# Kernel optimization log

Measured on AMD Instinct MI355X. Metric: run time of the kernel, lower is better.

Reference implementation:

```python
import jax, jax.numpy as jnp
import numpy as np

B, T, S, E, H, D = 4, 1024, 1024, 1024, 16, 64


def _ln(x, g, b, eps=1e-5):
    m = x.mean(-1, keepdims=True)
    v = ((x - m) ** 2).mean(-1, keepdims=True)
    return (x - m) * jax.lax.rsqrt(v + eps) * g + b


def _mha(xq, xkv, mask4, Wq, Wk, Wv, Wo, bo):
    # Wq/Wk/Wv: [H, E, D] (stacked per-head bias-free linears)
    q = jnp.einsum('bte,hed->bhtd', xq, Wq)
    k = jnp.einsum('bse,hed->bhsd', xkv, Wk)
    v = jnp.einsum('bse,hed->bhsd', xkv, Wv)
    # NOTE: original scales by C**-0.5 with C = n_embd, not head_size
    wei = jnp.einsum('bhtd,bhsd->bhts', q, k) * (float(E) ** -0.5)
    wei = jnp.where(mask4 == 0, jnp.float32(-1e9), wei)
    wei = jax.nn.softmax(wei, axis=-1)
    o = jnp.einsum('bhts,bhsd->bhtd', wei, v)  # [B,H,T,D]
    b_, h_, t_, d_ = o.shape
    o = o.transpose(0, 2, 1, 3).reshape(b_, t_, h_ * d_)
    return o @ Wo + bo


def setup_inputs() -> dict:
    key = jax.random.key(0)
    ks = jax.random.split(key, 24)
    sd = 0.02
    inp = {
        'x': jax.random.normal(ks[0], (B, T, E), jnp.float32),
        'x_m': jnp.ones((B, 1, T), jnp.int32),
        'ca': jax.random.normal(ks[1], (B, S, E), jnp.float32),
        'ca_m': jnp.ones((B, 1, S), jnp.int32),
        'Wq_s': jax.random.normal(ks[2], (H, E, D), jnp.float32) * sd,
        'Wk_s': jax.random.normal(ks[3], (H, E, D), jnp.float32) * sd,
        'Wv_s': jax.random.normal(ks[4], (H, E, D), jnp.float32) * sd,
        'Wo_s': jax.random.normal(ks[5], (E, E), jnp.float32) * sd,
        'bo_s': jnp.zeros((E,), jnp.float32),
        'Wq_c': jax.random.normal(ks[6], (H, E, D), jnp.float32) * sd,
        'Wk_c': jax.random.normal(ks[7], (H, E, D), jnp.float32) * sd,
        'Wv_c': jax.random.normal(ks[8], (H, E, D), jnp.float32) * sd,
        'Wo_c': jax.random.normal(ks[9], (E, E), jnp.float32) * sd,
        'bo_c': jnp.zeros((E,), jnp.float32),
        'ln1_g': jnp.ones((E,), jnp.float32), 'ln1_b': jnp.zeros((E,), jnp.float32),
        'ln2_g': jnp.ones((E,), jnp.float32), 'ln2_b': jnp.zeros((E,), jnp.float32),
        'ln3_g': jnp.ones((E,), jnp.float32), 'ln3_b': jnp.zeros((E,), jnp.float32),
        'W1': jax.random.normal(ks[10], (E, 4 * E), jnp.float32) * sd,
        'b1': jnp.zeros((4 * E,), jnp.float32),
        'W2': jax.random.normal(ks[11], (4 * E, E), jnp.float32) * sd,
        'b2': jnp.zeros((E,), jnp.float32),
    }
    return inp


def reference(x, x_m, ca, ca_m, Wq_s, Wk_s, Wv_s, Wo_s, bo_s,
              Wq_c, Wk_c, Wv_c, Wo_c, bo_c,
              ln1_g, ln1_b, ln2_g, ln2_b, ln3_g, ln3_b,
              W1, b1, W2, b2):
    tril = jnp.tril(jnp.ones((T, T), jnp.int32))
    # self-attn mask: x_m [B,1,T] & tril [T,T] -> [B,1,T,T] (broadcast over heads)
    self_mask = x_m[:, :, None, :] * tril          # [B,1,T,T]
    cross_mask = ca_m[:, :, None, :]               # [B,1,1,S]
    x = x + _mha(_ln(x, ln1_g, ln1_b), _ln(x, ln1_g, ln1_b) if False else _ln(x, ln1_g, ln1_b), self_mask, Wq_s, Wk_s, Wv_s, Wo_s, bo_s)
    x = x + _mha(_ln(x, ln2_g, ln2_b), ca, cross_mask, Wq_c, Wk_c, Wv_c, Wo_c, bo_c)
    h = _ln(x, ln3_g, ln3_b)
    x = x + (jax.nn.relu(h @ W1 + b1) @ W2 + b2)
    return x
```

## Files before the change

kernel.cpp:

```cpp
#include <hip/hip_runtime.h>
#include <hip/hip_bf16.h>
#include <cstdint>
#include <cstddef>

typedef __attribute__((ext_vector_type(8))) short  s8v;
typedef __attribute__((ext_vector_type(4))) short  s4v;
typedef __attribute__((ext_vector_type(8))) __bf16 b8v;
typedef __attribute__((ext_vector_type(4))) float  f32x4;
typedef __attribute__((ext_vector_type(4))) unsigned u32x4;

#define SC2Q 0.0450843293f

__device__ __forceinline__ short f2bf(float f){
  unsigned u = __builtin_bit_cast(unsigned, f);
  unsigned r = (u + 0x7fffu + ((u >> 16) & 1u)) >> 16;
  return (short)(unsigned short)r;
}
__device__ __forceinline__ float bf2f(short s){
  return __builtin_bit_cast(float, ((unsigned)(unsigned short)s) << 16);
}

__device__ __forceinline__ f32x4 mfma16(s8v a, s8v b, f32x4 c){
  return __builtin_amdgcn_mfma_f32_16x16x32_bf16(
      __builtin_bit_cast(b8v, a), __builtin_bit_cast(b8v, b), c, 0, 0, 0);
}

__device__ __forceinline__ unsigned cvtpk(float a, float b){
  unsigned w;
  asm("v_cvt_pk_bf16_f32 %0, %1, %2" : "=v"(w) : "v"(a), "v"(b));
  return w;
}

__global__ __launch_bounds__(256)
void ln_k(const float* __restrict__ x, const float* __restrict__ g,
          const float* __restrict__ b, short* __restrict__ out)
{
  const int row = blockIdx.x, tid = threadIdx.x;
  const float4 v = ((const float4*)(x + (size_t)row*1024))[tid];
  float s  = v.x+v.y+v.z+v.w;
  float s2 = v.x*v.x+v.y*v.y+v.z*v.z+v.w*v.w;
  #pragma unroll
  for (int off=32; off; off>>=1){ s += __shfl_down(s, off); s2 += __shfl_down(s2, off); }
  __shared__ float red[8];
  const int wave = tid>>6, lane = tid&63;
  if (lane==0){ red[wave]=s; red[4+wave]=s2; }
  __syncthreads();
  s  = red[0]+red[1]+red[2]+red[3];
  s2 = red[4]+red[5]+red[6]+red[7];
  const float mean = s*(1.f/1024.f);
  const float rstd = rsqrtf(s2*(1.f/1024.f) - mean*mean + 1e-5f);
  const float4 gv = ((const float4*)g)[tid];
  const float4 bv = ((const float4*)b)[tid];
  s4v o;
  o[0] = f2bf((v.x-mean)*rstd*gv.x + bv.x);
  o[1] = f2bf((v.y-mean)*rstd*gv.y + bv.y);
  o[2] = f2bf((v.z-mean)*rstd*gv.z + bv.z);
  o[3] = f2bf((v.w-mean)*rstd*gv.w + bv.w);
  *(s4v*)(out + (size_t)row*1024 + tid*4) = o;
}

__global__ __launch_bounds__(256)
void cast_k(const float* __restrict__ in, short* __restrict__ out)
{
  const int i = blockIdx.x*256 + threadIdx.x;
  const float4 v = ((const float4*)in)[i];
  s4v o; o[0]=f2bf(v.x); o[1]=f2bf(v.y); o[2]=f2bf(v.z); o[3]=f2bf(v.w);
  ((s4v*)out)[i] = o;
}

__global__ __launch_bounds__(256)
void mkb_k(const int* __restrict__ xm, const int* __restrict__ cm,
           float* __restrict__ mbS, float* __restrict__ mbC)
{
  const int i = blockIdx.x*256 + threadIdx.x;
  mbS[i] = xm[i] ? 0.f : -1.5e9f;
  mbC[i] = cm[i] ? 0.f : -1.5e9f;
}

__global__ __launch_bounds__(256)
void tcast_k(const float* __restrict__ in, short* __restrict__ out, int E2, int D2)
{
  __shared__ float t[32][33];
  const int h  = blockIdx.z;
  const int e0 = blockIdx.x*32, d0 = blockIdx.y*32;
  const int tx = threadIdx.x & 31, ty = threadIdx.x >> 5;
  const float* ip = in + (size_t)h*E2*D2;
  #pragma unroll
  for (int r = ty; r < 32; r += 8)
    t[r][tx] = ip[(size_t)(e0+r)*D2 + d0 + tx];
  __syncthreads();
  short* op = out + (size_t)h*D2*E2;
  #pragma unroll
  for (int r = ty; r < 32; r += 8)
    op[(size_t)(d0+r)*E2 + e0 + tx] = f2bf(t[tx][r]);
}

__global__ __launch_bounds__(256)
void vtrans_k(const short* __restrict__ V, int ldv, short* __restrict__ Vt, int S, int H)
{
  __shared__ short t[32][34];
  const int bh = blockIdx.z;
  const int b = bh / H, h = bh % H;
  const int s0 = blockIdx.x*32, d0 = blockIdx.y*32;
  const int tx = threadIdx.x & 31, ty = threadIdx.x >> 5;
  const short* ip = V + (size_t)b*S*ldv + h*64;
  #pragma unroll
  for (int r = ty; r < 32; r += 8)
    t[r][tx] = ip[(size_t)(s0+r)*ldv + d0 + tx];
  __syncthreads();
  const int s  = s0 + tx;
  const int ks = (s>>5)&1, bb = (tx>>4)&1, hh = (tx>>2)&3, rr = tx&3;
  const int cp = (s & ~63) + ks*32 + hh*8 + bb*4 + rr;
  short* op = Vt + ((size_t)bh*64 + d0)*S;
  #pragma unroll
  for (int r = ty; r < 32; r += 8)
    op[(size_t)r*S + cp] = t[tx][r];
}

__global__ __launch_bounds__(256)
void red4_k(const short* __restrict__ p, const float* __restrict__ bias,
            const float* __restrict__ resid, float* __restrict__ out)
{
  const int i = blockIdx.x*256 + threadIdx.x;
  float4 o = ((const float4*)resid)[i];
  const float4 bv = ((const float4*)bias)[i & 255];
  o.x += bv.x; o.y += bv.y; o.z += bv.z; o.w += bv.w;
  #pragma unroll
  for (int z=0; z<4; z++){
    const s4v v = ((const s4v*)(p + (size_t)z*4194304))[i];
    o.x += bf2f(v[0]); o.y += bf2f(v[1]); o.z += bf2f(v[2]); o.w += bf2f(v[3]);
  }
  ((float4*)out)[i] = o;
}

template<int BN, int BIAS, int RELU, int RESID, int WF32, int SCQ>
__global__ __launch_bounds__(256, 2)
void gemm_bt(const short* __restrict__ A, const short* __restrict__ Bt,
             const float* __restrict__ bias, const float* __restrict__ resid,
             short* __restrict__ Cb, float* __restrict__ Cf,
             int M, int N, int K)
{
  __shared__ short lds[3][128*32 + BN*32];
  const int nwg = gridDim.x * gridDim.y;
  int id = blockIdx.y * gridDim.x + blockIdx.x;
  id = (id & 7) * (nwg >> 3) + (id >> 3);
  const int bx = id % gridDim.x, by = id / gridDim.x;
  const int m0 = by*128, n0 = bx*BN;

  const int tid  = threadIdx.x;
  const int wave = tid>>6, lane = tid&63;
  const int lo = lane&15, hi = lane>>4;
  const int wm = wave>>1, wn = wave&1;

  constexpr int NJ = BN/32;
  constexpr int BC = BN>>6;
  f32x4 acc[4][NJ] = {};
  const int NK = K >> 5;

  auto stage = [&](int buf, int kt){
    const short* Ag = A  + (size_t)m0*K + kt*32;
    const short* Bg = Bt + (size_t)n0*K + kt*32;
    #pragma unroll
    for (int c=0;c<2;c++){
      const int q = (wave*2+c)*64 + lane;
      const int r = q>>2, cc = q&3;
      __builtin_amdgcn_global_load_lds(
        (const __attribute__((address_space(1))) void*)(Ag + (size_t)r*K + cc*8),
        (__attribute__((address_space(3))) void*)(&lds[buf][(wave*2+c)*512]),
        16, 0, 0);
    }
    #pragma unroll
    for (int c=0;c<BC;c++){
      const int q = (wave*BC+c)*64 + lane;
      const int r = q>>2, cc = q&3;
      __builtin_amdgcn_global_load_lds(
        (const __attribute__((address_space(1))) void*)(Bg + (size_t)r*K + cc*8),
        (__attribute__((address_space(3))) void*)(&lds[buf][4096 + (wave*BC+c)*512]),
        16, 0, 0);
    }
  };

  stage(0, 0);
  if (NK > 1) stage(1, 1);

  for (int kt=0; kt<NK; kt++){
    if (kt+1 < NK){
      if constexpr (BN==128) asm volatile("s_waitcnt vmcnt(4)" ::: "memory");
      else                   asm volatile("s_waitcnt vmcnt(3)" ::: "memory");
    } else {
      asm volatile("s_waitcnt vmcnt(0)" ::: "memory");
    }
    __builtin_amdgcn_s_barrier();
    __builtin_amdgcn_sched_barrier(0);
    if (kt+2 < NK) stage((kt+2)%3, kt+2);

    const short* la = &lds[kt%3][0];
    const short* lb = &lds[kt%3][4096];
    s8v af[4], bfr[NJ];
    #pragma unroll
    for (int i=0;i<4;i++)
      af[i] = *(const s8v*)(la + (wm*64 + i*16 + lo)*32 + hi*8);
    #pragma unroll
    for (int j=0;j<NJ;j++)
      bfr[j] = *(const s8v*)(lb + (wn*(BN/2) + j*16 + lo)*32 + hi*8);
    #pragma unroll
    for (int i=0;i<4;i++)
      #pragma unroll
      for (int j=0;j<NJ;j++)
        acc[i][j] = mfma16(af[i], bfr[j], acc[i][j]);
  }

  #pragma unroll
  for (int i=0;i<4;i++){
    const int row = m0 + wm*64 + i*16 + hi*4;
    #pragma unroll
    for (int j=0;j<NJ;j++){
      const int col = n0 + wn*(BN/2) + j*16 + lo;
      const float bv = BIAS ? bias[col] : 0.0f;
      #pragma unroll
      for (int r=0;r<4;r++){
        float v = acc[i][j][r] + bv;
        if constexpr (SCQ==2) v *= SC2Q;
        if (RELU) v = fmaxf(v, 0.0f);
        const size_t idx = (size_t)(row + r)*N + col;
        if (RESID) v += resid[idx];
        if (WF32) Cf[idx] = v; else Cb[idx] = f2bf(v);
      }
    }
  }
}

template<int BIAS, int RELU, int RESID, int WF32, int SCQ>
__global__ __launch_bounds__(512, 1)
void gemm256(const short* __restrict__ A, int lda,
             const short* __restrict__ Bt, int ldb,
             const float* __restrict__ bias, const float* __restrict__ resid,
             short* __restrict__ Cb, float* __restrict__ Cf,
             int M, int N, int K)
{
  __shared__ short lds[2][32768];
  const int nwg = gridDim.x * gridDim.y;
  int id = blockIdx.y * gridDim.x + blockIdx.x;
  id = (id & 7) * (nwg >> 3) + (id >> 3);
  const int bx = id % gridDim.x, by = id / gridDim.x;
  const int m0 = by*256, n0 = bx*256;
  A  += (size_t)blockIdx.z * K;
  Bt += (size_t)blockIdx.z * K;
  const size_t cofs = (size_t)blockIdx.z * M * N;

  const int tid = threadIdx.x;
  const int lane = tid&63, wave = tid>>6;
  const int lo = lane&15, hi = lane>>4;
  const int wr = wave>>2, wc = wave&3;

  f32x4 acc[8][4] = {};
  const int NT = K >> 6;

  auto stageA = [&](int buf, int kt, int part){
    const short* Ag = A + (size_t)m0*lda + kt*64;
    const int q = part*512 + tid;
    const int r = q>>3, c = q&7;
    __builtin_amdgcn_global_load_lds(
      (const __attribute__((address_space(1))) void*)(Ag + (size_t)r*lda + ((c^(r&7))*8)),
      (__attribute__((address_space(3))) void*)(&lds[buf][q*8]), 16, 0, 0);
  };
  auto stageB = [&](int buf, int kt, int part){
    const short* Bg = Bt + (size_t)n0*ldb + kt*64;
    const int q = part*512 + tid;
    const int r = q>>3, c = q&7;
    __builtin_amdgcn_global_load_lds(
      (const __attribute__((address_space(1))) void*)(Bg + (size_t)r*ldb + ((c^(r&7))*8)),
      (__attribute__((address_space(3))) void*)(&lds[buf][16384 + q*8]), 16, 0, 0);
  };

  #pragma unroll
  for (int p=0;p<4;p++){ stageA(0,0,p); stageB(0,0,p); }
  __syncthreads();

  for (int t=0; t<NT; t++){
    const int cur = t&1;
    const short* la = &lds[cur][0];
    const short* lb = &lds[cur][16384];
    const bool pf = (t+1 < NT);
    #pragma unroll
    for (int ks=0; ks<2; ks++){
      s8v bf[4];
      #pragma unroll
      for (int j=0;j<4;j++){
        const int r = wc*64 + j*16 + lo;
        bf[j] = *(const s8v*)(lb + r*64 + (((ks*4+hi)^(r&7))*8));
      }
      #pragma unroll
      for (int mh=0; mh<2; mh++){
        s8v af[4];
        #pragma unroll
        for (int i=0;i<4;i++){
          const int r = wr*128 + mh*64 + i*16 + lo;
          af[i] = *(const s8v*)(la + r*64 + (((ks*4+hi)^(r&7))*8));
        }
        if (pf && ks==0){
          stageA(cur^1, t+1, mh*2);   stageB(cur^1, t+1, mh*2);
          stageA(cur^1, t+1, mh*2+1); stageB(cur^1, t+1, mh*2+1);
        }
        __builtin_amdgcn_s_setprio(1);
        #pragma unroll
        for (int i=0;i<4;i++)
          #pragma unroll
          for (int j=0;j<4;j++)
            acc[mh*4+i][j] = mfma16(af[i], bf[j], acc[mh*4+i][j]);
        __builtin_amdgcn_s_setprio(0);
      }
    }
    __syncthreads();
  }

  #pragma unroll
  for (int I=0;I<8;I++){
    const int row = m0 + wr*128 + I*16 + hi*4;
    #pragma unroll
    for (int j=0;j<4;j++){
      const int col = n0 + wc*64 + j*16 + lo;
      const float bv = BIAS ? bias[col] : 0.0f;
      #pragma unroll
      for (int r=0;r<4;r++){
        float v = acc[I][j][r] + bv;
        if constexpr (SCQ==1) { if (col < 1024) v *= SC2Q; }
        if (RELU) v = fmaxf(v, 0.0f);
        const size_t idx = cofs + (size_t)(row + r)*N + col;
        if (RESID) v += resid[idx];
        if (WF32) Cf[idx] = v; else Cb[idx] = f2bf(v);
      }
    }
  }
}

template<int CAUSAL>
__global__ __launch_bounds__(256, 4)
void attn_k(const short* __restrict__ Q, int ldq,
            const short* __restrict__ K, int ldk,
            const short* __restrict__ Vt, int ldvt,
            const float* __restrict__ mbias,
            short* __restrict__ O, int ldo,
            int H, int Tq, int Sk)
{
  __shared__ short kls[2][4096];
  __shared__ short vls[2][4096];
  const int bh = blockIdx.x;
  const int b = bh / H, h = bh % H;
  const int tid = threadIdx.x;
  const int wave = tid>>6, lane = tid&63;
  const int lo = lane&15, hi = lane>>4;
  const int t0 = blockIdx.y*64 + wave*16;

  const short* Qb  = Q + (size_t)(b*Tq)*ldq + h*64;
  const short* Kb  = K + (size_t)(b*Sk)*ldk + h*64;
  const short* Vtb = Vt + (size_t)bh*64*ldvt;
  const float* mb  = mbias + (size_t)b*Sk;

  const short* qp = Qb + (size_t)(t0+lo)*ldq + hi*8;
  const s8v qa0 = *(const s8v*)(qp);
  const s8v qa1 = *(const s8v*)(qp + 32);

  float mrow = -INFINITY, lrow = 0.f;
  f32x4 oacc[4] = {};
  const int trow = t0 + lo;
  const int nblk = CAUSAL ? (blockIdx.y + 1) : (Sk>>6);
  const int x8 = lo & 7;

  auto stage = [&](int buf, int it){
    const int s0 = it*64;
    #pragma unroll
    for (int rd=0; rd<2; rd++){
      const int q = rd*256 + tid;
      const int r = q>>3, c = q&7;
      const int cs = (c ^ (r&7))*8;
      __builtin_amdgcn_global_load_lds(
        (const __attribute__((address_space(1))) void*)(Kb + (size_t)(s0+r)*ldk + cs),
        (__attribute__((address_space(3))) void*)(&kls[buf][(rd*256 + wave*64)*8]),
        16, 0, 0);
      __builtin_amdgcn_global_load_lds(
        (const __attribute__((address_space(1))) void*)(Vtb + (size_t)r*ldvt + s0 + cs),
        (__attribute__((address_space(3))) void*)(&vls[buf][(rd*256 + wave*64)*8]),
        16, 0, 0);
    }
  };

  stage(0, 0);
  int cur = 0;
  for (int it=0; it<nblk; it++){
    __syncthreads();
    if (it+1 < nblk) stage(cur^1, it+1);
    const int s0 = it*64;

    const short* kl = kls[cur];
    s8v kf[4][2];
    #pragma unroll
    for (int g=0; g<4; g++){
      const int rb = (g*16 + lo)*64;
      kf[g][0] = *(const s8v*)(kl + rb + ((hi     ^ x8)*8));
      kf[g][1] = *(const s8v*)(kl + rb + (((4+hi) ^ x8)*8));
    }

    f32x4 sg[4] = {};
    __builtin_amdgcn_s_setprio(1);
    #pragma unroll
    for (int g=0; g<4; g++){
      sg[g] = mfma16(kf[g][0], qa0, sg[g]);
      sg[g] = mfma16(kf[g][1], qa1, sg[g]);
    }
    __builtin_amdgcn_s_setprio(0);

    float p[4][4];
    #pragma unroll
    for (int g=0; g<4; g++){
      const f32x4 mv = ((const f32x4*)mb)[(s0>>2) + g*4 + hi];
      #pragma unroll
      for (int r=0; r<4; r++)
        p[g][r] = sg[g][r] + mv[r];
    }
    if (CAUSAL && it == nblk-1){
      #pragma unroll
      for (int g=0; g<4; g++)
        #pragma unroll
        for (int r=0; r<4; r++){
          const int sidx = s0 + g*16 + 4*hi + r;
          if (sidx > trow) p[g][r] = -1.5e9f;
        }
    }

    float bmax;
    {
      const float m0_ = fmaxf(fmaxf(fmaxf(p[0][0],p[0][1]),p[0][2]),p[0][3]);
      const float m1_ = fmaxf(fmaxf(fmaxf(p[1][0],p[1][1]),p[1][2]),p[1][3]);
      const float m2_ = fmaxf(fmaxf(fmaxf(p[2][0],p[2][1]),p[2][2]),p[2][3]);
      const float m3_ = fmaxf(fmaxf(fmaxf(p[3][0],p[3][1]),p[3][2]),p[3][3]);
      bmax = fmaxf(fmaxf(m0_,m1_), fmaxf(m2_,m3_));
    }
    bmax = fmaxf(bmax, __shfl_xor(bmax, 16));
    bmax = fmaxf(bmax, __shfl_xor(bmax, 32));

    if (!__all(bmax <= mrow + 8.0f)){
      const float mn  = fmaxf(mrow, bmax);
      const float fac = exp2f(mrow - mn);
      mrow = mn;
      lrow *= fac;
      #pragma unroll
      for (int f=0; f<4; f++)
        #pragma unroll
        for (int r=0; r<4; r++)
          oacc[f][r] *= fac;
    }

    float bsum;
    {
      #pragma unroll
      for (int g=0; g<4; g++)
        #pragma unroll
        for (int r=0; r<4; r++)
          p[g][r] = exp2f(p[g][r] - mrow);
      const float s0_ = (p[0][0]+p[0][1]) + (p[0][2]+p[0][3]);
      const float s1_ = (p[1][0]+p[1][1]) + (p[1][2]+p[1][3]);
      const float s2_ = (p[2][0]+p[2][1]) + (p[2][2]+p[2][3]);
      const float s3_ = (p[3][0]+p[3][1]) + (p[3][2]+p[3][3]);
      bsum = (s0_+s1_) + (s2_+s3_);
    }
    bsum += __shfl_xor(bsum, 16);
    bsum += __shfl_xor(bsum, 32);
    lrow += bsum;

    u32x4 pw0, pw1;
    pw0[0] = cvtpk(p[0][0], p[0][1]);
    pw0[1] = cvtpk(p[0][2], p[0][3]);
    pw0[2] = cvtpk(p[1][0], p[1][1]);
    pw0[3] = cvtpk(p[1][2], p[1][3]);
    pw1[0] = cvtpk(p[2][0], p[2][1]);
    pw1[1] = cvtpk(p[2][2], p[2][3]);
    pw1[2] = cvtpk(p[3][0], p[3][1]);
    pw1[3] = cvtpk(p[3][2], p[3][3]);
    const s8v pb0 = __builtin_bit_cast(s8v, pw0);
    const s8v pb1 = __builtin_bit_cast(s8v, pw1);

    const short* vl = vls[cur];
    __builtin_amdgcn_s_setprio(1);
    #pragma unroll
    for (int f=0; f<4; f++){
      const int rb = (f*16 + lo)*64;
      const s8v av0 = *(const s8v*)(vl + rb + (((hi  ) ^ x8)*8));
      const s8v av1 = *(const s8v*)(vl + rb + (((4+hi) ^ x8)*8));
      oacc[f] = mfma16(av0, pb0, oacc[f]);
      oacc[f] = mfma16(av1, pb1, oacc[f]);
    }
    __builtin_amdgcn_s_setprio(0);
    cur ^= 1;
  }

  const float inv = 1.0f / lrow;
  short* Ob = O + (size_t)(b*Tq)*ldo + h*64 + (size_t)(t0+lo)*ldo + 4*hi;
  #pragma unroll
  for (int f=0; f<4; f++){
    s4v o;
    #pragma unroll
    for (int r=0; r<4; r++) o[r] = f2bf(oacc[f][r]*inv);
    *(s4v*)(Ob + f*16) = o;
  }
}

extern "C" void kernel_launch(void* const* d_in, const int* in_sizes, int n_in,
                              void* d_out, int out_size, void* d_ws, size_t ws_size,
                              hipStream_t stream)
{
  (void)in_sizes; (void)n_in; (void)out_size; (void)ws_size;
  const float* x    = (const float*)d_in[0];
  const int*   xm   = (const int*)  d_in[1];
  const float* ca   = (const float*)d_in[2];
  const int*   cam  = (const int*)  d_in[3];
  const float* Wq_s = (const float*)d_in[4];
  const float* Wk_s = (const float*)d_in[5];
  const float* Wv_s = (const float*)d_in[6];
  const float* Wo_s = (const float*)d_in[7];
  const float* bo_s = (const float*)d_in[8];
  const float* Wq_c = (const float*)d_in[9];
  const float* Wk_c = (const float*)d_in[10];
  const float* Wv_c = (const float*)d_in[11];
  const float* Wo_c = (const float*)d_in[12];
  const float* bo_c = (const float*)d_in[13];
  const float* ln1g = (const float*)d_in[14];
  const float* ln1b = (const float*)d_in[15];
  const float* ln2g = (const float*)d_in[16];
  const float* ln2b = (const float*)d_in[17];
  const float* ln3g = (const float*)d_in[18];
  const float* ln3b = (const float*)d_in[19];
  const float* W1   = (const float*)d_in[20];
  const float* b1   = (const float*)d_in[21];
  const float* W2   = (const float*)d_in[22];
  const float* b2   = (const float*)d_in[23];
  float* out = (float*)d_out;

  char* ws = (char*)d_ws;
  size_t off = 0;
  auto alloc = [&](size_t bytes)->void*{
    void* p = ws + off; off += (bytes + 255) & ~(size_t)255; return p; };

  short* w_qkv_s = (short*)alloc((size_t)3072*1024*2);
  short* w_o_s   = (short*)alloc((size_t)1024*1024*2);
  short* w_q_c   = (short*)alloc((size_t)1024*1024*2);
  short* w_kv_c  = (short*)alloc((size_t)2048*1024*2);
  short* w_o_c   = (short*)alloc((size_t)1024*1024*2);
  short* w_1     = (short*)alloc((size_t)4096*1024*2);
  short* w_2     = (short*)alloc((size_t)1024*4096*2);
  short* xn      = (short*)alloc((size_t)4096*1024*2);
  short* cab     = (short*)alloc((size_t)4096*1024*2);
  short* qkv     = (short*)alloc((size_t)4096*3072*2);
  short* attno   = (short*)alloc((size_t)4096*1024*2);
  float* xres    = (float*)alloc((size_t)4096*1024*4);
  short* hffn    = (short*)alloc((size_t)4096*4096*2);
  float* pA      = (float*)alloc((size_t)4096*1024*4);
  float* pB      = (float*)alloc((size_t)4096*1024*4);
  float* mbS     = (float*)alloc((size_t)4096*4);
  float* mbC     = (float*)alloc((size_t)4096*4);
  short* pP      = (short*)pA;
  short* kvbuf   = qkv + (size_t)4096*1024;
  short* vt_s    = hffn;
  short* vt_c    = hffn + (size_t)4*1024*1024;
  (void)pB;

  tcast_k<<<dim3(32,  2,16),256,0,stream>>>(Wq_s, w_qkv_s,           1024,   64);
  tcast_k<<<dim3(32,  2,16),256,0,stream>>>(Wk_s, w_qkv_s+1024*1024, 1024,   64);
  tcast_k<<<dim3(32,  2,16),256,0,stream>>>(Wv_s, w_qkv_s+2048*1024, 1024,   64);
  tcast_k<<<dim3(32, 32, 1),256,0,stream>>>(Wo_s, w_o_s,             1024, 1024);
  tcast_k<<<dim3(32,  2,16),256,0,stream>>>(Wq_c, w_q_c,             1024,   64);
  tcast_k<<<dim3(32,  2,16),256,0,stream>>>(Wk_c, w_kv_c,            1024,   64);
  tcast_k<<<dim3(32,  2,16),256,0,stream>>>(Wv_c, w_kv_c+1024*1024,  1024,   64);
  tcast_k<<<dim3(32, 32, 1),256,0,stream>>>(Wo_c, w_o_c,             1024, 1024);
  tcast_k<<<dim3(32,128, 1),256,0,stream>>>(W1,   w_1,               1024, 4096);
  tcast_k<<<dim3(128,32, 1),256,0,stream>>>(W2,   w_2,               4096, 1024);
  cast_k<<<4096,256,0,stream>>>(ca, cab);
  mkb_k<<<16,256,0,stream>>>(xm, cam, mbS, mbC);

  ln_k<<<4096,256,0,stream>>>(x, ln1g, ln1b, xn);
  gemm256<0,0,0,0,1><<<dim3(12,16),512,0,stream>>>(xn, 1024, w_qkv_s, 1024,
                                                   nullptr, nullptr, qkv, nullptr,
                                                   4096, 3072, 1024);
  vtrans_k<<<dim3(32,2,64),256,0,stream>>>(qkv+2048, 3072, vt_s, 1024, 16);
  attn_k<1><<<dim3(64,16),256,0,stream>>>(qkv, 3072, qkv+1024, 3072, vt_s, 1024,
                                          mbS, attno, 1024, 16, 1024, 1024);
  gemm_bt<64,1,0,1,1,0><<<dim3(16,32),256,0,stream>>>(attno, w_o_s, bo_s, x,
                                                      nullptr, xres, 4096, 1024, 1024);

  ln_k<<<4096,256,0,stream>>>(xres, ln2g, ln2b, xn);
  gemm_bt<64,0,0,0,0,2><<<dim3(16,32),256,0,stream>>>(xn, w_q_c, nullptr, nullptr,
                                                      qkv, nullptr, 4096, 1024, 1024);
  gemm256<0,0,0,0,0><<<dim3(8,16),512,0,stream>>>(cab, 1024, w_kv_c, 1024,
                                                  nullptr, nullptr, kvbuf, nullptr,
                                                  4096, 2048, 1024);
  vtrans_k<<<dim3(32,2,64),256,0,stream>>>(kvbuf+1024, 2048, vt_c, 1024, 16);
  attn_k<0><<<dim3(64,16),256,0,stream>>>(qkv, 1024, kvbuf, 2048, vt_c, 1024,
                                          mbC, attno, 1024, 16, 1024, 1024);
  gemm_bt<64,1,0,1,1,0><<<dim3(16,32),256,0,stream>>>(attno, w_o_c, bo_c, xres,
                                                      nullptr, xres, 4096, 1024, 1024);

  ln_k<<<4096,256,0,stream>>>(xres, ln3g, ln3b, xn);
  gemm256<1,1,0,0,0><<<dim3(16,16),512,0,stream>>>(xn, 1024, w_1, 1024,
                                                   b1, nullptr, hffn, nullptr,
                                                   4096, 4096, 1024);
  gemm256<0,0,0,0,0><<<dim3(4,16,4),512,0,stream>>>(hffn, 4096, w_2, 4096,
                                                    nullptr, nullptr, pP, nullptr,
                                                    4096, 1024, 1024);
  red4_k<<<4096,256,0,stream>>>(pP, b2, xres, out);
}
```

Measured before the change: 368.0 us.

## Compute softmax row sums via MFMA with ones vector and precompute staging addresses

Replaces the per-iteration VALU summation and cross-lane shuffles for the softmax denominator with two extra MFMAs that multiply a bf16 ones vector by the probability fragments, accumulating the row sum in a matrix accumulator. It also hoists the global-to-LDS staging addresses into incrementing pointers, and uses byte-offset LDS addressing and a pointer-advanced mask bias load. The max reduction is reordered into a flatter tree. This trades shuffles and scalar adds for extra matrix-core work, and the denominator now sums bf16-rounded probabilities, which slightly changes numerics.

New measurement: 362.4 us. No clear change (-1.5%).

```diff
diff --git a/kernel.cpp b/kernel.cpp
--- a/kernel.cpp
+++ b/kernel.cpp
@@ -355,50 +355,66 @@
   const short* Qb  = Q + (size_t)(b*Tq)*ldq + h*64;
   const short* Kb  = K + (size_t)(b*Sk)*ldk + h*64;
   const short* Vtb = Vt + (size_t)bh*64*ldvt;
-  const float* mb  = mbias + (size_t)b*Sk;
 
   const short* qp = Qb + (size_t)(t0+lo)*ldq + hi*8;
   const s8v qa0 = *(const s8v*)(qp);
   const s8v qa1 = *(const s8v*)(qp + 32);
 
-  float mrow = -INFINITY, lrow = 0.f;
+  float mrow = -INFINITY;
   f32x4 oacc[4] = {};
+  f32x4 oaccL = {};
   const int trow = t0 + lo;
   const int nblk = CAUSAL ? (blockIdx.y + 1) : (Sk>>6);
   const int x8 = lo & 7;
 
-  auto stage = [&](int buf, int it){
-    const int s0 = it*64;
-    #pragma unroll
-    for (int rd=0; rd<2; rd++){
-      const int q = rd*256 + tid;
-      const int r = q>>3, c = q&7;
-      const int cs = (c ^ (r&7))*8;
-      __builtin_amdgcn_global_load_lds(
-        (const __attribute__((address_space(1))) void*)(Kb + (size_t)(s0+r)*ldk + cs),
-        (__attribute__((address_space(3))) void*)(&kls[buf][(rd*256 + wave*64)*8]),
-        16, 0, 0);
-      __builtin_amdgcn_global_load_lds(
-        (const __attribute__((address_space(1))) void*)(Vtb + (size_t)r*ldvt + s0 + cs),
-        (__attribute__((address_space(3))) void*)(&vls[buf][(rd*256 + wave*64)*8]),
-        16, 0, 0);
-    }
+  const s8v onesv = {(short)0x3F80,(short)0x3F80,(short)0x3F80,(short)0x3F80,
+                     (short)0x3F80,(short)0x3F80,(short)0x3F80,(short)0x3F80};
+
+  const int q0 = tid, q1 = 256 + tid;
+  const int r0 = q0>>3, cs0 = ((q0&7) ^ (r0&7))*8;
+  const int r1 = q1>>3, cs1 = ((q1&7) ^ (r1&7))*8;
+  const short* kS0 = Kb + (size_t)r0*ldk + cs0;
+  const short* kS1 = Kb + (size_t)r1*ldk + cs1;
+  const short* vS0 = Vtb + (size_t)r0*ldvt + cs0;
+  const short* vS1 = Vtb + (size_t)r1*ldvt + cs1;
+  const size_t kAdv = (size_t)64*ldk;
+
+  auto stage = [&](int buf){
+    __builtin_amdgcn_global_load_lds(
+      (const __attribute__((address_space(1))) void*)kS0,
+      (__attribute__((address_space(3))) void*)(&kls[buf][wave*512]), 16, 0, 0);
+    __builtin_amdgcn_global_load_lds(
+      (const __attribute__((address_space(1))) void*)kS1,
+      (__attribute__((address_space(3))) void*)(&kls[buf][2048 + wave*512]), 16, 0, 0);
+    __builtin_amdgcn_global_load_lds(
+      (const __attribute__((address_space(1))) void*)vS0,
+      (__attribute__((address_space(3))) void*)(&vls[buf][wave*512]), 16, 0, 0);
+    __builtin_amdgcn_global_load_lds(
+      (const __attribute__((address_space(1))) void*)vS1,
+      (__attribute__((address_space(3))) void*)(&vls[buf][2048 + wave*512]), 16, 0, 0);
+    kS0 += kAdv; kS1 += kAdv; vS0 += 64; vS1 += 64;
   };
 
-  stage(0, 0);
-  int cur = 0;
+  const char* klsB = (const char*)kls;
+  const char* vlsB = (const char*)vls;
+  const int A0 = lo*128 + ((hi     ^ x8)*16);
+  const int A1 = lo*128 + (((4+hi) ^ x8)*16);
+  int curB = 0;
+
+  const char* mbp = (const char*)(mbias + (size_t)b*Sk) + hi*16;
+
+  stage(0);
   for (int it=0; it<nblk; it++){
     __syncthreads();
-    if (it+1 < nblk) stage(cur^1, it+1);
-    const int s0 = it*64;
-
-    const short* kl = kls[cur];
+    if (it+1 < nblk) stage((it+1)&1);
+
+    const char* ka0 = klsB + curB + A0;
+    const char* ka1 = klsB + curB + A1;
     s8v kf[4][2];
     #pragma unroll
     for (int g=0; g<4; g++){
-      const int rb = (g*16 + lo)*64;
-      kf[g][0] = *(const s8v*)(kl + rb + ((hi     ^ x8)*8));
-      kf[g][1] = *(const s8v*)(kl + rb + (((4+hi) ^ x8)*8));
+      kf[g][0] = *(const s8v*)(ka0 + g*2048);
+      kf[g][1] = *(const s8v*)(ka1 + g*2048);
     }
 
     f32x4 sg[4] = {};
@@ -413,12 +429,14 @@
     float p[4][4];
     #pragma unroll
     for (int g=0; g<4; g++){
-      const f32x4 mv = ((const f32x4*)mb)[(s0>>2) + g*4 + hi];
+      const f32x4 mv = *(const f32x4*)(mbp + g*64);
       #pragma unroll
       for (int r=0; r<4; r++)
         p[g][r] = sg[g][r] + mv[r];
     }
+    mbp += 256;
     if (CAUSAL && it == nblk-1){
+      const int s0 = it*64;
       #pragma unroll
       for (int g=0; g<4; g++)
         #pragma unroll
@@ -430,11 +448,12 @@
 
     float bmax;
     {
-      const float m0_ = fmaxf(fmaxf(fmaxf(p[0][0],p[0][1]),p[0][2]),p[0][3]);
-      const float m1_ = fmaxf(fmaxf(fmaxf(p[1][0],p[1][1]),p[1][2]),p[1][3]);
-      const float m2_ = fmaxf(fmaxf(fmaxf(p[2][0],p[2][1]),p[2][2]),p[2][3]);
-      const float m3_ = fmaxf(fmaxf(fmaxf(p[3][0],p[3][1]),p[3][2]),p[3][3]);
-      bmax = fmaxf(fmaxf(m0_,m1_), fmaxf(m2_,m3_));
+      const float m0_ = fmaxf(fmaxf(p[0][0],p[0][1]),p[0][2]);
+      const float m1_ = fmaxf(fmaxf(p[0][3],p[1][0]),p[1][1]);
+      const float m2_ = fmaxf(fmaxf(p[1][2],p[1][3]),p[2][0]);
+      const float m3_ = fmaxf(fmaxf(p[2][1],p[2][2]),p[2][3]);
+      const float m4_ = fmaxf(fmaxf(p[3][0],p[3][1]),p[3][2]);
+      bmax = fmaxf(fmaxf(fmaxf(m0_,m1_),m2_), fmaxf(fmaxf(m3_,m4_),p[3][3]));
     }
     bmax = fmaxf(bmax, __shfl_xor(bmax, 16));
     bmax = fmaxf(bmax, __shfl_xor(bmax, 32));
@@ -443,30 +462,20 @@
       const float mn  = fmaxf(mrow, bmax);
       const float fac = exp2f(mrow - mn);
       mrow = mn;
-      lrow *= fac;
       #pragma unroll
       for (int f=0; f<4; f++)
         #pragma unroll
         for (int r=0; r<4; r++)
           oacc[f][r] *= fac;
-    }
-
-    float bsum;
-    {
-      #pragma unroll
-      for (int g=0; g<4; g++)
-        #pragma unroll
-        for (int r=0; r<4; r++)
-          p[g][r] = exp2f(p[g][r] - mrow);
-      const float s0_ = (p[0][0]+p[0][1]) + (p[0][2]+p[0][3]);
-      const float s1_ = (p[1][0]+p[1][1]) + (p[1][2]+p[1][3]);
-      const float s2_ = (p[2][0]+p[2][1]) + (p[2][2]+p[2][3]);
-      const float s3_ = (p[3][0]+p[3][1]) + (p[3][2]+p[3][3]);
-      bsum = (s0_+s1_) + (s2_+s3_);
-    }
-    bsum += __shfl_xor(bsum, 16);
-    bsum += __shfl_xor(bsum, 32);
-    lrow += bsum;
+      #pragma unroll
+      for (int r=0; r<4; r++) oaccL[r] *= fac;
+    }
+
+    #pragma unroll
+    for (int g=0; g<4; g++)
+      #pragma unroll
+      for (int r=0; r<4; r++)
+        p[g][r] = exp2f(p[g][r] - mrow);
 
     u32x4 pw0, pw1;
     pw0[0] = cvtpk(p[0][0], p[0][1]);
@@ -480,21 +489,23 @@
     const s8v pb0 = __builtin_bit_cast(s8v, pw0);
     const s8v pb1 = __builtin_bit_cast(s8v, pw1);
 
-    const short* vl = vls[cur];
+    const char* va0 = vlsB + curB + A0;
+    const char* va1 = vlsB + curB + A1;
     __builtin_amdgcn_s_setprio(1);
     #pragma unroll
     for (int f=0; f<4; f++){
-      const int rb = (f*16 + lo)*64;
-      const s8v av0 = *(const s8v*)(vl + rb + (((hi  ) ^ x8)*8));
-      const s8v av1 = *(const s8v*)(vl + rb + (((4+hi) ^ x8)*8));
+      const s8v av0 = *(const s8v*)(va0 + f*2048);
+      const s8v av1 = *(const s8v*)(va1 + f*2048);
       oacc[f] = mfma16(av0, pb0, oacc[f]);
       oacc[f] = mfma16(av1, pb1, oacc[f]);
     }
+    oaccL = mfma16(onesv, pb0, oaccL);
+    oaccL = mfma16(onesv, pb1, oaccL);
     __builtin_amdgcn_s_setprio(0);
-    cur ^= 1;
+    curB ^= 8192;
   }
 
-  const float inv = 1.0f / lrow;
+  const float inv = 1.0f / oaccL[0];
   short* Ob = O + (size_t)(b*Tq)*ldo + h*64 + (size_t)(t0+lo)*ldo + 4*hi;
   #pragma unroll
   for (int f=0; f<4; f++){
```
